# Kernel optimization log

Hardware: AMD Instinct MI355X
Metric: run time of the kernel (lower is better)

## Reference

```python
import jax, jax.numpy as jnp
import numpy as np

H, D, DK, DV = 8, 512, 64, 64
EPS = 1e-5


def layer_norm(x, g, b):
    mu = jnp.mean(x, axis=-1, keepdims=True)
    var = jnp.var(x, axis=-1, keepdims=True)
    return (x - mu) * jax.lax.rsqrt(var + EPS) * g + b


def setup_inputs() -> dict:
    key = jax.random.key(0)
    ks = jax.random.split(key, 12)
    B, L = 4, 2048
    q = jax.random.normal(ks[0], (B, L, D), jnp.float32)
    k = jax.random.normal(ks[1], (B, L, D), jnp.float32)
    v = jax.random.normal(ks[2], (B, L, D), jnp.float32)
    mask = jax.random.randint(ks[3], (H * B, L), 0, 2, jnp.int32)
    std_qk = np.sqrt(2.0 / (D + DK))
    std_v = np.sqrt(2.0 / (D + DV))
    Wq = jax.random.normal(ks[4], (H * DK, D), jnp.float32) * std_qk
    Wk = jax.random.normal(ks[5], (H * DK, D), jnp.float32) * std_qk
    Wv = jax.random.normal(ks[6], (H * DV, D), jnp.float32) * std_v
    fc_w = jax.random.normal(ks[7], (D, H * DV), jnp.float32) * np.sqrt(2.0 / (D + H * DV))
    fc_b = jnp.zeros((D,), jnp.float32)
    g0 = jnp.ones((D,), jnp.float32)
    b0 = jnp.zeros((D,), jnp.float32)
    g1 = jnp.ones((D,), jnp.float32)
    b1 = jnp.zeros((D,), jnp.float32)
    return {"q": q, "k": k, "v": v, "mask": mask, "Wq": Wq, "Wk": Wk,
            "Wv": Wv, "fc_w": fc_w, "fc_b": fc_b, "g0": g0, "b0": b0,
            "g1": g1, "b1": b1}


def reference(q, k, v, mask, Wq, Wk, Wv, fc_w, fc_b, g0, b0, g1, b1):
    B, Lq, _ = q.shape
    Lk = k.shape[1]
    temperature = np.power(DK, 0.5)
    residual = q
    # projections -> [H*B, L, dk/dv] matching torch permute(2,0,1,3).view(-1, L, d)
    qh = (q @ Wq.T).reshape(B, Lq, H, DK).transpose(2, 0, 1, 3).reshape(H * B, Lq, DK)
    kh = (k @ Wk.T).reshape(B, Lk, H, DK).transpose(2, 0, 1, 3).reshape(H * B, Lk, DK)
    vh = (v @ Wv.T).reshape(B, Lk, H, DV).transpose(2, 0, 1, 3).reshape(H * B, Lk, DV)
    attn = jnp.einsum('nqd,nkd->nqk', qh, kh)  # [H*B, Lq, Lk]
    attn = jnp.where(mask[:, None, :] == 0, jnp.float32(-1e9), attn)
    attn = attn / temperature
    attn = jax.nn.softmax(attn, axis=2)  # dropout is identity in eval
    out = jnp.einsum('nqk,nkd->nqd', attn, vh)  # [H*B, Lq, DV]
    out = out.reshape(H, B, Lq, DV).transpose(1, 2, 0, 3).reshape(B, Lq, H * DV)
    out = layer_norm(out + residual, g0, b0)
    new_residual = out
    out = out @ fc_w.T + fc_b
    out = layer_norm(out + new_residual, g1, b1)
    return out
```

## Files before the change

### kernel.cpp

```cpp
#include <hip/hip_runtime.h>
#include <hip/hip_bf16.h>

typedef __bf16 bf16;
typedef bf16 bf16x8 __attribute__((ext_vector_type(8)));
typedef bf16 bf16x4 __attribute__((ext_vector_type(4)));
typedef float f32x4 __attribute__((ext_vector_type(4)));

#define MFMA16(a,b,c) __builtin_amdgcn_mfma_f32_16x16x32_bf16(a,b,c,0,0,0)

__device__ inline void gload_lds16(const bf16* g, bf16* l) {
  __builtin_amdgcn_global_load_lds(
      (const __attribute__((address_space(1))) unsigned int*)g,
      (__attribute__((address_space(3))) unsigned int*)l,
      16, 0, 0);
}

__device__ inline bf16x8 ldsfrag(const bf16* base, int r, int cb) {
  return *(const bf16x8*)(base + r*64 + ((cb ^ (r & 7)) << 3));
}

__global__ __launch_bounds__(256) void cvt_kernel(
    const float* __restrict__ q, const float* __restrict__ k_, const float* __restrict__ v,
    const float* __restrict__ Wq, const float* __restrict__ Wk, const float* __restrict__ Wv,
    const float* __restrict__ fcw,
    bf16* __restrict__ qb, bf16* __restrict__ kb, bf16* __restrict__ vb,
    bf16* __restrict__ Wqb, bf16* __restrict__ Wkb, bf16* __restrict__ Wvb,
    bf16* __restrict__ fcwb)
{
  const int y = blockIdx.y;
  const float* src; bf16* dst; int n;
  if      (y==0) { src=q;   dst=qb;   n=4194304; }
  else if (y==1) { src=k_;  dst=kb;   n=4194304; }
  else if (y==2) { src=v;   dst=vb;   n=4194304; }
  else if (y==3) { src=Wq;  dst=Wqb;  n=262144;  }
  else if (y==4) { src=Wk;  dst=Wkb;  n=262144;  }
  else if (y==5) { src=Wv;  dst=Wvb;  n=262144;  }
  else           { src=fcw; dst=fcwb; n=262144;  }
  const int i = (blockIdx.x*256 + threadIdx.x)*4;
  if (i >= n) return;
  f32x4 x = *(const f32x4*)(src + i);
  bf16x4 o;
  o[0]=(bf16)x[0]; o[1]=(bf16)x[1]; o[2]=(bf16)x[2]; o[3]=(bf16)x[3];
  *(bf16x4*)(dst + i) = o;
}

__global__ __launch_bounds__(256) void proj_kernel(
    const bf16* __restrict__ qb, const bf16* __restrict__ kb, const bf16* __restrict__ vb,
    const bf16* __restrict__ Wqb, const bf16* __restrict__ Wkb, const bf16* __restrict__ Wvb,
    bf16* __restrict__ qh, bf16* __restrict__ kh, bf16* __restrict__ vhT)
{
  const int p = blockIdx.z;
  const bf16* A = (p==0)?qb:(p==1)?kb:vb;
  const bf16* W = (p==0)?Wqb:(p==1)?Wkb:Wvb;
  const int m0 = blockIdx.x*128, n0 = blockIdx.y*64;
  const int l  = threadIdx.x & 63, w = threadIdx.x >> 6;
  const int lr = l & 15, lh = l >> 4;

  __shared__ bf16 sA[2][8192];
  __shared__ bf16 sW[2][4096];

  auto stageA = [&](bf16* d, int kk) {
#pragma unroll
    for (int c = 0; c < 4; ++c) {
      const int i   = (w*4 + c)*64 + l;
      const int r   = i >> 3;
      const int cbs = (i & 7) ^ (r & 7);
      gload_lds16(A + (size_t)(m0 + r)*512 + kk + cbs*8, d + (w*4+c)*512);
    }
  };
  auto stageW = [&](bf16* d, int kk) {
#pragma unroll
    for (int c = 0; c < 2; ++c) {
      const int i   = (w*2 + c)*64 + l;
      const int r   = i >> 3;
      const int cbs = (i & 7) ^ (r & 7);
      gload_lds16(W + (size_t)(n0 + r)*512 + kk + cbs*8, d + (w*2+c)*512);
    }
  };

  stageA(sA[0], 0); stageW(sW[0], 0);
  __syncthreads();

  f32x4 zero = {0.f,0.f,0.f,0.f};
  f32x4 acc[2][4] = {{zero,zero,zero,zero},{zero,zero,zero,zero}};

  int cur = 0;
#pragma unroll 1
  for (int kk = 0; kk < 512; kk += 64) {
    if (kk + 64 < 512) { stageA(sA[cur^1], kk+64); stageW(sW[cur^1], kk+64); }
    const bf16* a_ = sA[cur];
    const bf16* w_ = sW[cur];
#pragma unroll
    for (int s = 0; s < 2; ++s) {
      bf16x8 a0 = ldsfrag(a_, w*32 + lr,      s*4 + lh);
      bf16x8 a1 = ldsfrag(a_, w*32 + 16 + lr, s*4 + lh);
#pragma unroll
      for (int t = 0; t < 4; ++t) {
        bf16x8 wf = ldsfrag(w_, t*16 + lr, s*4 + lh);
        acc[0][t] = MFMA16(a0, wf, acc[0][t]);
        acc[1][t] = MFMA16(a1, wf, acc[1][t]);
      }
    }
    __syncthreads();
    cur ^= 1;
  }

  const float qscale = 0.18033688011112042f;
#pragma unroll
  for (int g = 0; g < 2; ++g)
#pragma unroll
    for (int t = 0; t < 4; ++t) {
      const int ncol = n0 + t*16 + lr;
      const int h = ncol >> 6, d = ncol & 63;
#pragma unroll
      for (int j = 0; j < 4; ++j) {
        const int m   = m0 + w*32 + g*16 + lh*4 + j;
        const int b   = m >> 11, tok = m & 2047;
        float val = acc[g][t][j];
        if (p == 0) val *= qscale;
        const bf16 bv = (bf16)val;
        if (p == 0)      qh [((size_t)((h<<2)|b)*2048 + tok)*64 + d]   = bv;
        else if (p == 1) kh [((size_t)((h<<2)|b)*2048 + tok)*64 + d]   = bv;
        else             vhT[((size_t)((h<<2)|b)*64   + d)*2048 + tok] = bv;
      }
    }
}

__global__ __launch_bounds__(256, 3) void attn_kernel(
    const bf16* __restrict__ qh, const bf16* __restrict__ kh, const bf16* __restrict__ vhT,
    const int* __restrict__ mask, float* __restrict__ attn_out)
{
  const int n  = blockIdx.y;
  const int w  = threadIdx.x >> 6;
  const int l  = threadIdx.x & 63;
  const int lr = l & 15, lh = l >> 4;
  const int q0 = blockIdx.x*128 + w*32;
  const bf16* qn = qh  + (size_t)n*2048*64;
  const bf16* kn = kh  + (size_t)n*2048*64;
  const bf16* vn = vhT + (size_t)n*64*2048;
  const int h = n >> 2, b = n & 3;

  __shared__ float smask[2048];
  __shared__ bf16  sK[2][4096];
  __shared__ bf16  sV[2][4096];
  __shared__ bf16  sP[4][16][72];

  auto stage = [&](bf16* dK, bf16* dV, int kt_) {
#pragma unroll
    for (int c = 0; c < 2; ++c) {
      const int i   = (w*2 + c)*64 + l;
      const int r   = i >> 3;
      const int cbs = (i & 7) ^ (r & 7);
      gload_lds16(kn + (size_t)(kt_ + r)*64   + cbs*8, dK + (w*2+c)*512);
      gload_lds16(vn + (size_t)r*2048 + kt_   + cbs*8, dV + (w*2+c)*512);
    }
  };

  {
    const int* mn = mask + n*2048;
    const int i0 = (int)threadIdx.x * 8;
    int4 m0v = *(const int4*)(mn + i0);
    int4 m1v = *(const int4*)(mn + i0 + 4);
    f32x4 f0, f1;
    f0[0]=m0v.x?1.f:0.f; f0[1]=m0v.y?1.f:0.f; f0[2]=m0v.z?1.f:0.f; f0[3]=m0v.w?1.f:0.f;
    f1[0]=m1v.x?1.f:0.f; f1[1]=m1v.y?1.f:0.f; f1[2]=m1v.z?1.f:0.f; f1[3]=m1v.w?1.f:0.f;
    *(f32x4*)(smask + i0)     = f0;
    *(f32x4*)(smask + i0 + 4) = f1;
  }
  stage(sK[0], sV[0], 0);
  __syncthreads();

  bf16x8 aq[2][2];
#pragma unroll
  for (int g = 0; g < 2; ++g) {
    aq[g][0] = *(const bf16x8*)(qn + (size_t)(q0+g*16+lr)*64 + lh*8);
    aq[g][1] = *(const bf16x8*)(qn + (size_t)(q0+g*16+lr)*64 + 32 + lh*8);
  }

  f32x4 zero = {0.f,0.f,0.f,0.f};
  f32x4 acc[2][4] = {{zero,zero,zero,zero},{zero,zero,zero,zero}};
  float ssum[2][4] = {{0.f,0.f,0.f,0.f},{0.f,0.f,0.f,0.f}};

  int cur = 0;
#pragma unroll 1
  for (int kt = 0; kt < 2048; kt += 64) {
    const int ktn = kt + 64;
    if (ktn < 2048) stage(sK[cur^1], sV[cur^1], ktn);

    const bf16* sKc = sK[cur];
    const bf16* sVc = sV[cur];

    f32x4 sc[2][4] = {{zero,zero,zero,zero},{zero,zero,zero,zero}};
#pragma unroll
    for (int t = 0; t < 4; ++t) {
      bf16x8 bk0 = ldsfrag(sKc, t*16 + lr, lh);
      bf16x8 bk1 = ldsfrag(sKc, t*16 + lr, lh + 4);
      sc[0][t] = MFMA16(aq[0][0], bk0, sc[0][t]);
      sc[0][t] = MFMA16(aq[0][1], bk1, sc[0][t]);
      sc[1][t] = MFMA16(aq[1][0], bk0, sc[1][t]);
      sc[1][t] = MFMA16(aq[1][1], bk1, sc[1][t]);
    }
#pragma unroll
    for (int t = 0; t < 4; ++t) {
      const float msk = smask[kt + t*16 + lr];
#pragma unroll
      for (int g = 0; g < 2; ++g)
#pragma unroll
        for (int j = 0; j < 4; ++j) {
          const float e = exp2f(fminf(sc[g][t][j], 100.f)) * msk;
          sc[g][t][j] = e;
          ssum[g][j] += e;
        }
    }
    bf16x8 vf0[4], vf1[4];
#pragma unroll
    for (int dt = 0; dt < 4; ++dt) {
      vf0[dt] = ldsfrag(sVc, dt*16 + lr, lh);
      vf1[dt] = ldsfrag(sVc, dt*16 + lr, lh + 4);
    }
#pragma unroll
    for (int g = 0; g < 2; ++g) {
#pragma unroll
      for (int t = 0; t < 4; ++t)
#pragma unroll
        for (int j = 0; j < 4; ++j)
          sP[w][lh*4 + j][t*16 + lr] = (bf16)sc[g][t][j];
      asm volatile("s_waitcnt lgkmcnt(0)" ::: "memory");
      __builtin_amdgcn_sched_barrier(0);
      bf16x8 pa0 = *(const bf16x8*)(&sP[w][lr][lh*8]);
      bf16x8 pa1 = *(const bf16x8*)(&sP[w][lr][32 + lh*8]);
#pragma unroll
      for (int dt = 0; dt < 4; ++dt) {
        acc[g][dt] = MFMA16(pa0, vf0[dt], acc[g][dt]);
        acc[g][dt] = MFMA16(pa1, vf1[dt], acc[g][dt]);
      }
    }
    __syncthreads();
    cur ^= 1;
  }

#pragma unroll
  for (int off = 1; off < 16; off <<= 1)
#pragma unroll
    for (int g = 0; g < 2; ++g)
#pragma unroll
      for (int j = 0; j < 4; ++j)
        ssum[g][j] += __shfl_xor(ssum[g][j], off, 16);
#pragma unroll
  for (int g = 0; g < 2; ++g) {
    float inv[4];
#pragma unroll
    for (int j = 0; j < 4; ++j) inv[j] = (ssum[g][j] > 0.f) ? 1.f/ssum[g][j] : 0.f;
#pragma unroll
    for (int dt = 0; dt < 4; ++dt)
#pragma unroll
      for (int j = 0; j < 4; ++j) {
        const int tok = q0 + g*16 + lh*4 + j;
        const int dv  = dt*16 + lr;
        attn_out[((size_t)(b*2048 + tok))*512 + h*64 + dv] = acc[g][dt][j]*inv[j];
      }
  }
}

__global__ __launch_bounds__(256) void ln_kernel(
    const float* xa, const float* xb,
    const float* __restrict__ g, const float* __restrict__ bb,
    float* outf, bf16* outb)
{
  const int row = blockIdx.x*4 + (threadIdx.x >> 6);
  const int l   = threadIdx.x & 63;
  const float* pa = xa + (size_t)row*512;
  const float* pb = xb + (size_t)row*512;
  f32x4 u0 = *(const f32x4*)(pa + 4*l);
  f32x4 u1 = *(const f32x4*)(pa + 256 + 4*l);
  f32x4 w0 = *(const f32x4*)(pb + 4*l);
  f32x4 w1 = *(const f32x4*)(pb + 256 + 4*l);
  u0 = u0 + w0; u1 = u1 + w1;
  float s = 0.f, sq = 0.f;
#pragma unroll
  for (int e = 0; e < 4; ++e) { s += u0[e] + u1[e]; sq += u0[e]*u0[e] + u1[e]*u1[e]; }
#pragma unroll
  for (int off = 1; off < 64; off <<= 1) {
    s  += __shfl_xor(s,  off, 64);
    sq += __shfl_xor(sq, off, 64);
  }
  const float mean = s * (1.f/512.f);
  const float var  = fmaxf(sq * (1.f/512.f) - mean*mean, 0.f);
  const float r    = rsqrtf(var + 1e-5f);
  f32x4 g0v = *(const f32x4*)(g + 4*l),  g1v = *(const f32x4*)(g + 256 + 4*l);
  f32x4 b0v = *(const f32x4*)(bb + 4*l), b1v = *(const f32x4*)(bb + 256 + 4*l);
  f32x4 o0, o1;
#pragma unroll
  for (int e = 0; e < 4; ++e) {
    o0[e] = (u0[e] - mean)*r*g0v[e] + b0v[e];
    o1[e] = (u1[e] - mean)*r*g1v[e] + b1v[e];
  }
  *(f32x4*)(outf + (size_t)row*512 + 4*l)       = o0;
  *(f32x4*)(outf + (size_t)row*512 + 256 + 4*l) = o1;
  if (outb) {
    bf16x4 ob0, ob1;
#pragma unroll
    for (int e = 0; e < 4; ++e) { ob0[e]=(bf16)o0[e]; ob1[e]=(bf16)o1[e]; }
    *(bf16x4*)(outb + (size_t)row*512 + 4*l)       = ob0;
    *(bf16x4*)(outb + (size_t)row*512 + 256 + 4*l) = ob1;
  }
}

__global__ __launch_bounds__(256) void fc_kernel(
    const bf16* __restrict__ A, const bf16* __restrict__ W,
    const float* __restrict__ bias, float* __restrict__ out)
{
  const int m0 = blockIdx.x*128, n0 = blockIdx.y*64;
  const int l  = threadIdx.x & 63, w = threadIdx.x >> 6;
  const int lr = l & 15, lh = l >> 4;

  __shared__ bf16 sA[2][8192];
  __shared__ bf16 sW[2][4096];

  auto stageA = [&](bf16* d, int kk) {
#pragma unroll
    for (int c = 0; c < 4; ++c) {
      const int i   = (w*4 + c)*64 + l;
      const int r   = i >> 3;
      const int cbs = (i & 7) ^ (r & 7);
      gload_lds16(A + (size_t)(m0 + r)*512 + kk + cbs*8, d + (w*4+c)*512);
    }
  };
  auto stageW = [&](bf16* d, int kk) {
#pragma unroll
    for (int c = 0; c < 2; ++c) {
      const int i   = (w*2 + c)*64 + l;
      const int r   = i >> 3;
      const int cbs = (i & 7) ^ (r & 7);
      gload_lds16(W + (size_t)(n0 + r)*512 + kk + cbs*8, d + (w*2+c)*512);
    }
  };

  stageA(sA[0], 0); stageW(sW[0], 0);
  __syncthreads();

  f32x4 zero = {0.f,0.f,0.f,0.f};
  f32x4 acc[2][4] = {{zero,zero,zero,zero},{zero,zero,zero,zero}};

  int cur = 0;
#pragma unroll 1
  for (int kk = 0; kk < 512; kk += 64) {
    if (kk + 64 < 512) { stageA(sA[cur^1], kk+64); stageW(sW[cur^1], kk+64); }
    const bf16* a_ = sA[cur];
    const bf16* w_ = sW[cur];
#pragma unroll
    for (int s = 0; s < 2; ++s) {
      bf16x8 a0 = ldsfrag(a_, w*32 + lr,      s*4 + lh);
      bf16x8 a1 = ldsfrag(a_, w*32 + 16 + lr, s*4 + lh);
#pragma unroll
      for (int t = 0; t < 4; ++t) {
        bf16x8 wf = ldsfrag(w_, t*16 + lr, s*4 + lh);
        acc[0][t] = MFMA16(a0, wf, acc[0][t]);
        acc[1][t] = MFMA16(a1, wf, acc[1][t]);
      }
    }
    __syncthreads();
    cur ^= 1;
  }

#pragma unroll
  for (int g = 0; g < 2; ++g)
#pragma unroll
    for (int t = 0; t < 4; ++t) {
      const int ncol = n0 + t*16 + lr;
      const float bs = bias[ncol];
#pragma unroll
      for (int j = 0; j < 4; ++j) {
        const int m = m0 + w*32 + g*16 + lh*4 + j;
        out[(size_t)m*512 + ncol] = acc[g][t][j] + bs;
      }
    }
}

extern "C" void kernel_launch(void* const* d_in, const int* in_sizes, int n_in,
                              void* d_out, int out_size, void* d_ws, size_t ws_size,
                              hipStream_t stream) {
  const float* q    = (const float*)d_in[0];
  const float* k    = (const float*)d_in[1];
  const float* v    = (const float*)d_in[2];
  const int*   mask = (const int*)  d_in[3];
  const float* Wq   = (const float*)d_in[4];
  const float* Wk   = (const float*)d_in[5];
  const float* Wv   = (const float*)d_in[6];
  const float* fcw  = (const float*)d_in[7];
  const float* fcb  = (const float*)d_in[8];
  const float* g0   = (const float*)d_in[9];
  const float* b0   = (const float*)d_in[10];
  const float* g1   = (const float*)d_in[11];
  const float* b1   = (const float*)d_in[12];

  char* ws = (char*)d_ws;
  bf16*  qb   = (bf16*) (ws);
  bf16*  kb   = (bf16*) (ws + (8ull  << 20));
  bf16*  vb   = (bf16*) (ws + (16ull << 20));
  bf16*  Wqb  = (bf16*) (ws + (24ull << 20));
  bf16*  Wkb  = (bf16*) (ws + (24ull << 20) + (512ull << 10));
  bf16*  Wvb  = (bf16*) (ws + (25ull << 20));
  bf16*  fcwb = (bf16*) (ws + (25ull << 20) + (512ull << 10));
  bf16*  qh   = (bf16*) (ws + (26ull << 20));
  bf16*  kh   = (bf16*) (ws + (34ull << 20));
  bf16*  vhT  = (bf16*) (ws + (42ull << 20));
  float* attnb= (float*)(ws);
  float* x1   = (float*)(ws + (26ull << 20));
  bf16*  x1b  = (bf16*) (ws + (50ull << 20));
  float* out  = (float*)d_out;

  cvt_kernel <<<dim3(4096, 7), 256, 0, stream>>>(q, k, v, Wq, Wk, Wv, fcw,
                                                 qb, kb, vb, Wqb, Wkb, Wvb, fcwb);
  proj_kernel<<<dim3(64, 8, 3), 256, 0, stream>>>(qb, kb, vb, Wqb, Wkb, Wvb, qh, kh, vhT);
  attn_kernel<<<dim3(16, 32),   256, 0, stream>>>(qh, kh, vhT, mask, attnb);
  ln_kernel  <<<2048,           256, 0, stream>>>(attnb, q, g0, b0, x1, x1b);
  fc_kernel  <<<dim3(64, 8),    256, 0, stream>>>(x1b, fcwb, fcb, out);
  ln_kernel  <<<2048,           256, 0, stream>>>(out, x1, g1, b1, out, nullptr);
}
```

Baseline: 156.6 us.

## Transpose QK^T MFMA to keep P in registers, dropping LDS round-trip

Swaps the operand order of the QK^T MFMA so each lane holds scores in the layout needed as the A operand of a 16x16x16 bf16 MFMA for PV. Probabilities are packed directly into registers instead of being written to and re-read from a per-wave LDS scratch, removing the sP buffer, its waitcnt and sched barrier. Row sums are now per-lane across keys and are reduced with cross-row shuffles. The PV product uses the smaller-K MFMA with narrower 8-byte LDS reads of V, so it issues more instructions per tile.

```diff
diff --git a/kernel.cpp b/kernel.cpp
--- a/kernel.cpp
+++ b/kernel.cpp
@@ -5,8 +5,11 @@
 typedef bf16 bf16x8 __attribute__((ext_vector_type(8)));
 typedef bf16 bf16x4 __attribute__((ext_vector_type(4)));
 typedef float f32x4 __attribute__((ext_vector_type(4)));
-
-#define MFMA16(a,b,c) __builtin_amdgcn_mfma_f32_16x16x32_bf16(a,b,c,0,0,0)
+typedef short s16x4 __attribute__((ext_vector_type(4)));
+typedef unsigned u32x2 __attribute__((ext_vector_type(2)));
+
+#define MFMA16(a,b,c)   __builtin_amdgcn_mfma_f32_16x16x32_bf16(a,b,c,0,0,0)
+#define MFMA1616(a,b,c) __builtin_amdgcn_mfma_f32_16x16x16bf16_1k(a,b,c,0,0,0)
 
 __device__ inline void gload_lds16(const bf16* g, bf16* l) {
   __builtin_amdgcn_global_load_lds(
@@ -17,6 +20,16 @@
 
 __device__ inline bf16x8 ldsfrag(const bf16* base, int r, int cb) {
   return *(const bf16x8*)(base + r*64 + ((cb ^ (r & 7)) << 3));
+}
+
+__device__ inline unsigned pack2(float lo, float hi) {
+  unsigned short a = __builtin_bit_cast(unsigned short, (bf16)lo);
+  unsigned short b = __builtin_bit_cast(unsigned short, (bf16)hi);
+  return (unsigned)a | ((unsigned)b << 16);
+}
+__device__ inline s16x4 mk4(unsigned lo, unsigned hi) {
+  u32x2 t; t[0] = lo; t[1] = hi;
+  return __builtin_bit_cast(s16x4, t);
 }
 
 __global__ __launch_bounds__(256) void cvt_kernel(
@@ -143,7 +156,6 @@
   __shared__ float smask[2048];
   __shared__ bf16  sK[2][4096];
   __shared__ bf16  sV[2][4096];
-  __shared__ bf16  sP[4][16][72];
 
   auto stage = [&](bf16* dK, bf16* dV, int kt_) {
 #pragma unroll
@@ -179,7 +191,7 @@
 
   f32x4 zero = {0.f,0.f,0.f,0.f};
   f32x4 acc[2][4] = {{zero,zero,zero,zero},{zero,zero,zero,zero}};
-  float ssum[2][4] = {{0.f,0.f,0.f,0.f},{0.f,0.f,0.f,0.f}};
+  float ssum[2] = {0.f, 0.f};
 
   int cur = 0;
 #pragma unroll 1
@@ -195,44 +207,34 @@
     for (int t = 0; t < 4; ++t) {
       bf16x8 bk0 = ldsfrag(sKc, t*16 + lr, lh);
       bf16x8 bk1 = ldsfrag(sKc, t*16 + lr, lh + 4);
-      sc[0][t] = MFMA16(aq[0][0], bk0, sc[0][t]);
-      sc[0][t] = MFMA16(aq[0][1], bk1, sc[0][t]);
-      sc[1][t] = MFMA16(aq[1][0], bk0, sc[1][t]);
-      sc[1][t] = MFMA16(aq[1][1], bk1, sc[1][t]);
-    }
+      sc[0][t] = MFMA16(bk0, aq[0][0], sc[0][t]);
+      sc[0][t] = MFMA16(bk1, aq[0][1], sc[0][t]);
+      sc[1][t] = MFMA16(bk0, aq[1][0], sc[1][t]);
+      sc[1][t] = MFMA16(bk1, aq[1][1], sc[1][t]);
+    }
+    s16x4 pa[2][4];
 #pragma unroll
     for (int t = 0; t < 4; ++t) {
-      const float msk = smask[kt + t*16 + lr];
-#pragma unroll
-      for (int g = 0; g < 2; ++g)
-#pragma unroll
-        for (int j = 0; j < 4; ++j) {
-          const float e = exp2f(fminf(sc[g][t][j], 100.f)) * msk;
-          sc[g][t][j] = e;
-          ssum[g][j] += e;
-        }
-    }
-    bf16x8 vf0[4], vf1[4];
-#pragma unroll
-    for (int dt = 0; dt < 4; ++dt) {
-      vf0[dt] = ldsfrag(sVc, dt*16 + lr, lh);
-      vf1[dt] = ldsfrag(sVc, dt*16 + lr, lh + 4);
-    }
-#pragma unroll
-    for (int g = 0; g < 2; ++g) {
-#pragma unroll
-      for (int t = 0; t < 4; ++t)
-#pragma unroll
-        for (int j = 0; j < 4; ++j)
-          sP[w][lh*4 + j][t*16 + lr] = (bf16)sc[g][t][j];
-      asm volatile("s_waitcnt lgkmcnt(0)" ::: "memory");
-      __builtin_amdgcn_sched_barrier(0);
-      bf16x8 pa0 = *(const bf16x8*)(&sP[w][lr][lh*8]);
-      bf16x8 pa1 = *(const bf16x8*)(&sP[w][lr][32 + lh*8]);
+      const f32x4 m4 = *(const f32x4*)(smask + kt + t*16 + lh*4);
+#pragma unroll
+      for (int g = 0; g < 2; ++g) {
+        float e0 = exp2f(fminf(sc[g][t][0], 100.f)) * m4[0];
+        float e1 = exp2f(fminf(sc[g][t][1], 100.f)) * m4[1];
+        float e2 = exp2f(fminf(sc[g][t][2], 100.f)) * m4[2];
+        float e3 = exp2f(fminf(sc[g][t][3], 100.f)) * m4[3];
+        ssum[g] += (e0 + e1) + (e2 + e3);
+        pa[g][t] = mk4(pack2(e0, e1), pack2(e2, e3));
+      }
+    }
+#pragma unroll
+    for (int t = 0; t < 4; ++t) {
+      const int cb = 2*t + (lh >> 1);
 #pragma unroll
       for (int dt = 0; dt < 4; ++dt) {
-        acc[g][dt] = MFMA16(pa0, vf0[dt], acc[g][dt]);
-        acc[g][dt] = MFMA16(pa1, vf1[dt], acc[g][dt]);
+        const int r = dt*16 + lr;
+        s16x4 vb = *(const s16x4*)(sVc + r*64 + ((cb ^ (r & 7)) << 3) + (lh & 1)*4);
+        acc[0][dt] = MFMA1616(pa[0][t], vb, acc[0][dt]);
+        acc[1][dt] = MFMA1616(pa[1][t], vb, acc[1][dt]);
       }
     }
     __syncthreads();
@@ -240,17 +242,18 @@
   }
 
 #pragma unroll
-  for (int off = 1; off < 16; off <<= 1)
-#pragma unroll
-    for (int g = 0; g < 2; ++g)
-#pragma unroll
-      for (int j = 0; j < 4; ++j)
-        ssum[g][j] += __shfl_xor(ssum[g][j], off, 16);
+  for (int g = 0; g < 2; ++g) {
+    ssum[g] += __shfl_xor(ssum[g], 16, 64);
+    ssum[g] += __shfl_xor(ssum[g], 32, 64);
+  }
 #pragma unroll
   for (int g = 0; g < 2; ++g) {
     float inv[4];
 #pragma unroll
-    for (int j = 0; j < 4; ++j) inv[j] = (ssum[g][j] > 0.f) ? 1.f/ssum[g][j] : 0.f;
+    for (int j = 0; j < 4; ++j) {
+      const float sq = __shfl(ssum[g], lh*4 + j, 16);
+      inv[j] = (sq > 0.f) ? 1.f/sq : 0.f;
+    }
 #pragma unroll
     for (int dt = 0; dt < 4; ++dt)
 #pragma unroll
```

Measured after the change: 157.1 us. Within noise of the previous version (+0.3%).
